# Kernel tuning notes

Measured on AMD Instinct MI355X. Metric: run time of the kernel, lower is better.

Reference implementation:

```python
import jax, jax.numpy as jnp
import numpy as np

# Module constants from init_kwargs
A, T, HID, H, EGO = 50, 50, 128, 32, 0
C = 4 * HID // H   # per-head out channels = 16
B = 32
NEG_SLOPE = 0.2    # PyG GATConv default negative_slope


def setup_inputs() -> dict:
    key = jax.random.key(0)
    k1, k2, k3, k4 = jax.random.split(key, 4)
    h = jax.random.normal(k1, (B, A, T, HID), dtype=jnp.float32)
    # GATConv params: lin.weight (H*C, HID), att_src/att_dst (H, C), bias (H*C,)
    W = jax.random.normal(k2, (H * C, HID), dtype=jnp.float32) * (1.0 / np.sqrt(HID))
    att_src = jax.random.normal(k3, (H, C), dtype=jnp.float32) * 0.1
    att_dst = jax.random.normal(k4, (H, C), dtype=jnp.float32) * 0.1
    bias = jnp.zeros((H * C,), dtype=jnp.float32)
    return {"h": h, "W": W, "att_src": att_src, "att_dst": att_dst, "bias": bias}


def reference(h, W, att_src, att_dst, bias):
    # h: (B, A, T, HID). Node id = t*A + a after permute, matching build_ego_star_edges.
    b = h.shape[0]
    x = jnp.transpose(h, (0, 2, 1, 3))                       # (B, T, A, HID)
    # Linear projection into heads: (B, T, A, H, C)
    xw = jnp.einsum('btad,hcd->btahc', x, W.reshape(H, C, HID))
    a_src = jnp.einsum('btahc,hc->btah', xw, att_src)        # per-node src logit
    a_dst = jnp.einsum('btahc,hc->btah', xw, att_dst)        # per-node dst logit

    # Star topology: every (t_src, a != EGO) node -> every (t_dst, EGO) node.
    ne = jnp.array([a for a in range(A) if a != EGO])        # (A-1,) non-ego agents
    S = T * (A - 1)                                          # neighbors per ego dst
    x_ne = xw[:, :, ne].reshape(b, S, H, C)                  # (B, S, H, C)
    a_src_ne = a_src[:, :, ne].reshape(b, S, H)              # (B, S, H)
    a_dst_ego = a_dst[:, :, EGO]                             # (B, T, H)

    # Per-edge attention logits, segment-softmax over the S neighbors of each dst.
    logits = jax.nn.leaky_relu(a_src_ne[:, None, :, :] + a_dst_ego[:, :, None, :],
                               negative_slope=NEG_SLOPE)     # (B, T, S, H)
    att = jax.nn.softmax(logits, axis=2)

    # Weighted aggregation: (B, T, H, C) -> flatten heads (concat=True)
    out_ego = jnp.einsum('btsh,bshc->bthc', att, x_ne).reshape(b, T, H * C)

    # Nodes with no incoming edges get zero aggregation; bias added to all.
    out = jnp.zeros((b, T, A, H * C), dtype=h.dtype).at[:, :, EGO].set(out_ego)
    out = out + bias
    return jnp.transpose(out, (0, 2, 1, 3))                  # (B, A, T, H*C)
```

## Files before the change

### kernel.cpp

```cpp
#include <hip/hip_runtime.h>
#include <math.h>

#define NA    50
#define NT    50
#define HIDK  128
#define NH    32
#define NC    16
#define NB    32
#define SAT   2500
#define NS    2450
#define NOUT  512

__global__ __launch_bounds__(256) void k0_pq(const float* __restrict__ W,
                                             const float* __restrict__ att_src,
                                             const float* __restrict__ att_dst,
                                             float* __restrict__ PQ) {
  int g = blockIdx.x * 256 + threadIdx.x;
  int j = g >> 7, k = g & 127;
  int hh = j & 31;
  const float* att = (j < 32) ? att_src : att_dst;
  float acc = 0.f;
  #pragma unroll
  for (int c = 0; c < 16; ++c)
    acc = fmaf(att[hh * 16 + c], W[(size_t)(hh * 16 + c) * 128 + k], acc);
  PQ[g] = acc;
}

__global__ __launch_bounds__(256) void k1_ud(
    const float* __restrict__ X,
    const float* __restrict__ PQ,
    float* __restrict__ u,
    float* __restrict__ dv)
{
  __shared__ float Ast[32][68];
  __shared__ float Bst[32][68];
  const int tid = threadIdx.x;
  const int m0 = blockIdx.x * 64;
  const int ty = tid >> 4, tx = tid & 15;
  float acc[4][4] = {};
  const int sr = tid >> 3, sc = tid & 7;

  for (int kc = 0; kc < 128; kc += 32) {
    #pragma unroll
    for (int L = 0; L < 2; ++L) {
      int row = sr + L * 32;
      float4 v = *(const float4*)&X[(size_t)(m0 + row) * 128 + kc + sc * 4];
      Ast[sc*4+0][row] = v.x; Ast[sc*4+1][row] = v.y;
      Ast[sc*4+2][row] = v.z; Ast[sc*4+3][row] = v.w;
      float4 w = *(const float4*)&PQ[(size_t)row * 128 + kc + sc * 4];
      Bst[sc*4+0][row] = w.x; Bst[sc*4+1][row] = w.y;
      Bst[sc*4+2][row] = w.z; Bst[sc*4+3][row] = w.w;
    }
    __syncthreads();
    #pragma unroll
    for (int k = 0; k < 32; ++k) {
      float4 a4 = *(const float4*)&Ast[k][ty * 4];
      float4 b4 = *(const float4*)&Bst[k][tx * 4];
      float a[4] = {a4.x, a4.y, a4.z, a4.w};
      float bb[4] = {b4.x, b4.y, b4.z, b4.w};
      #pragma unroll
      for (int i = 0; i < 4; ++i)
        #pragma unroll
        for (int j = 0; j < 4; ++j)
          acc[i][j] = fmaf(a[i], bb[j], acc[i][j]);
    }
    __syncthreads();
  }

  #pragma unroll
  for (int i = 0; i < 4; ++i) {
    int m = m0 + ty * 4 + i;
    int b = m / SAT, s = m - b * SAT;
    #pragma unroll
    for (int jj = 0; jj < 4; ++jj) {
      int col = tx * 4 + jj;
      if (col < 32)
        u[(size_t)(b * 32 + col) * SAT + s] = acc[i][jj];
      else if (s < NT)
        dv[(size_t)(b * 32 + col - 32) * NT + s] = acc[i][jj];
    }
  }
}

#define LOADG(B_, g_) do {                                                  \
    _Pragma("unroll")                                                       \
    for (int j = 0; j < 4; ++j) {                                           \
      int idx_ = base + 2 * ((g_) * 4 + j);                                 \
      e##B_[j] = sE[idx_]; s##B_[j] = sIdx[idx_];                           \
    }                                                                       \
    _Pragma("unroll")                                                       \
    for (int j = 0; j < 4; ++j)                                             \
      x##B_[j] = *(const float4*)(xb + (size_t)s##B_[j] * HIDK);            \
  } while (0)

#define COMPG(B_) do {                                                      \
    _Pragma("unroll")                                                       \
    for (int j = 0; j < 4; ++j) {                                           \
      float2 ee = e##B_[j]; float4 xx = x##B_[j];                           \
      a1[0]=fmaf(ee.x,xx.x,a1[0]); a1[1]=fmaf(ee.x,xx.y,a1[1]);             \
      a1[2]=fmaf(ee.x,xx.z,a1[2]); a1[3]=fmaf(ee.x,xx.w,a1[3]);             \
      a2[0]=fmaf(ee.y,xx.x,a2[0]); a2[1]=fmaf(ee.y,xx.y,a2[1]);             \
      a2[2]=fmaf(ee.y,xx.z,a2[2]); a2[3]=fmaf(ee.y,xx.w,a2[3]);             \
      z1 += ee.x; z2 += ee.y;                                               \
    }                                                                       \
  } while (0)

__global__ __launch_bounds__(512, 4) void k2_attn(
    const float* __restrict__ X,
    const float* __restrict__ u,
    const float* __restrict__ dv,
    const float* __restrict__ W,
    const float* __restrict__ bias,
    float* __restrict__ out)
{
  const int id = blockIdx.x;
  const int b  = (id & 7) + 8 * (id >> 8);
  const int h  = (id >> 3) & 31;
  const int tid = threadIdx.x;

  __shared__ float Bb[2][51][129];
  __shared__ float2 sE[NS];
  __shared__ unsigned short sIdx[NS];
  __shared__ float sTheta[50], sD[50], sF1[50], sF2[50];
  __shared__ int   sRank[50];
  __shared__ int   offs[52];
  __shared__ int   offCur[51];
  __shared__ int   segOrder[51];
  __shared__ int   segCtr;
  __shared__ float red[8];
  __shared__ float sMaxU;

  float* sU = &Bb[0][0][0];
  unsigned short* sBeta = (unsigned short*)&Bb[1][0][0];

  const size_t bh = (size_t)b * 32 + h;
  const float* uP = u + bh * SAT + NT;

  float mx = -1e30f;
  for (int i = tid; i < NS; i += 512) { float v = uP[i]; sU[i] = v; mx = fmaxf(mx, v); }
  if (tid < 50) sD[tid] = dv[bh * NT + tid];
  if (tid < 51) offCur[tid] = 0;
  #pragma unroll
  for (int o = 32; o; o >>= 1) mx = fmaxf(mx, __shfl_xor(mx, o));
  if ((tid & 63) == 0) red[tid >> 6] = mx;
  __syncthreads();
  if (tid == 0) {
    float m2 = red[0];
    #pragma unroll
    for (int k = 1; k < 8; ++k) m2 = fmaxf(m2, red[k]);
    sMaxU = m2;
  }
  __syncthreads();
  const float maxU = sMaxU;

  if (tid < 50) {
    float th = -sD[tid];
    int r = 0;
    for (int t2 = 0; t2 < 50; ++t2) {
      float th2 = -sD[t2];
      r += (th2 < th) || (th2 == th && t2 < tid);
    }
    sRank[tid] = r;
    sTheta[r] = th;
    float x = maxU + sD[tid];
    float L = (x >= 0.f) ? x : 0.2f * x;
    sF1[tid] = __expf(x - L);
    sF2[tid] = __expf(0.2f * x - L);
  }
  __syncthreads();

  for (int i = tid; i < NS; i += 512) {
    float uu = sU[i];
    int lo = 0, hi = 50;
    while (lo < hi) { int mid = (lo + hi) >> 1; if (sTheta[mid] <= uu) lo = mid + 1; else hi = mid; }
    sBeta[i] = (unsigned short)lo;
    atomicAdd(&offCur[lo], 1);
  }
  __syncthreads();

  if (tid < 64) {
    int c = (tid < 51) ? offCur[tid] : 0;
    int inc = c;
    #pragma unroll
    for (int o = 1; o < 64; o <<= 1) {
      int n = __shfl_up(inc, o);
      if (tid >= o) inc += n;
    }
    if (tid < 51) { int ex = inc - c; offs[tid] = ex; offCur[tid] = ex; }
    if (tid == 50) offs[51] = inc;
  }
  __syncthreads();

  if (tid < 51) {
    int sz = offs[tid + 1] - offs[tid];
    int r = 0;
    for (int t2 = 0; t2 < 51; ++t2) {
      int sz2 = offs[t2 + 1] - offs[t2];
      r += (sz2 > sz) || (sz2 == sz && t2 < tid);
    }
    segOrder[r] = tid;
  }
  if (tid == 511) segCtr = 0;
  for (int i = tid; i < NS; i += 512) {
    float uu = sU[i];
    int beta = sBeta[i];
    int pos = atomicAdd(&offCur[beta], 1);
    sE[pos] = make_float2(__expf(uu - maxU), __expf(0.2f * (uu - maxU)));
    sIdx[pos] = (unsigned short)(i + NT);
  }
  __syncthreads();

  {
    const int lane = tid & 63;
    const int slot = lane >> 5;
    const int cq   = lane & 31;
    const float* xb = X + (size_t)b * SAT * HIDK + cq * 4;

    for (;;) {
      int kidx = 0;
      if (lane == 0) kidx = atomicAdd(&segCtr, 1);
      kidx = __shfl(kidx, 0);
      if (kidx >= 51) break;
      const int seg = segOrder[kidx];

      const int i0 = offs[seg], i1 = offs[seg + 1];
      const int base = i0 + slot;
      int np = i1 - base;
      np = (np > 0) ? ((np + 1) >> 1) : 0;
      const int G = np >> 2;

      float a1[4] = {0.f, 0.f, 0.f, 0.f};
      float a2[4] = {0.f, 0.f, 0.f, 0.f};
      float z1 = 0.f, z2 = 0.f;

      float2 eA[4], eB[4]; int sA[4], sB[4]; float4 xA[4], xB[4];
      int g = 0;
      if (G) LOADG(A, 0);
      while (g + 2 <= G) {
        LOADG(B, g + 1);
        COMPG(A);
        if (g + 2 < G) LOADG(A, g + 2);
        COMPG(B);
        g += 2;
      }
      if (g < G) COMPG(A);
      for (int k = G * 4; k < np; ++k) {
        int idx = base + 2 * k;
        float2 ee = sE[idx];
        int ss = sIdx[idx];
        float4 xx = *(const float4*)(xb + (size_t)ss * HIDK);
        a1[0]=fmaf(ee.x,xx.x,a1[0]); a1[1]=fmaf(ee.x,xx.y,a1[1]);
        a1[2]=fmaf(ee.x,xx.z,a1[2]); a1[3]=fmaf(ee.x,xx.w,a1[3]);
        a2[0]=fmaf(ee.y,xx.x,a2[0]); a2[1]=fmaf(ee.y,xx.y,a2[1]);
        a2[2]=fmaf(ee.y,xx.z,a2[2]); a2[3]=fmaf(ee.y,xx.w,a2[3]);
        z1 += ee.x; z2 += ee.y;
      }

      #pragma unroll
      for (int j = 0; j < 4; ++j) {
        a1[j] += __shfl_xor(a1[j], 32);
        a2[j] += __shfl_xor(a2[j], 32);
      }
      z1 += __shfl_xor(z1, 32);
      z2 += __shfl_xor(z2, 32);
      if (slot == 0) {
        #pragma unroll
        for (int j = 0; j < 4; ++j) {
          Bb[0][seg][cq * 4 + j] = a1[j];
          Bb[1][seg][cq * 4 + j] = a2[j];
        }
        if (cq == 0) { Bb[0][seg][128] = z1; Bb[1][seg][128] = z2; }
      }
    }
  }
  __syncthreads();

  float* WshT = (float*)sE;
  const float* Wh = W + (size_t)h * 16 * 128;
  for (int v = tid; v < 2048; v += 512) {
    int k = v >> 4, cout = v & 15;
    WshT[k * 16 + cout] = Wh[(size_t)cout * 128 + k];
  }
  for (int task = tid; task < 258; task += 512) {
    int which = task >= 129;
    int c = task - which * 129;
    if (which == 0) {
      float run = 0.f;
      for (int k = 50; k >= 0; --k) { float tmp = Bb[0][k][c]; Bb[0][k][c] = run; run += tmp; }
    } else {
      float run = 0.f;
      for (int k = 0; k <= 50; ++k) { run += Bb[1][k][c]; Bb[1][k][c] = run; }
    }
  }
  __syncthreads();

  for (int task = tid; task < NT * NC; task += 512) {
    int t = task >> 4, cout = task & 15;
    int r = sRank[t];
    float F1 = sF1[t], F2 = sF2[t];
    float z = F1 * Bb[0][r][128] + F2 * Bb[1][r][128];
    const float* b1r = &Bb[0][r][0];
    const float* b2r = &Bb[1][r][0];
    float n1 = 0.f, n2 = 0.f;
    #pragma unroll 4
    for (int c = 0; c < 128; ++c) {
      float w = WshT[c * 16 + cout];
      n1 = fmaf(b1r[c], w, n1);
      n2 = fmaf(b2r[c], w, n2);
    }
    out[((size_t)b * SAT + t) * NOUT + h * 16 + cout] =
        (F1 * n1 + F2 * n2) / z + bias[h * 16 + cout];
  }

  {
    int g0 = id * 9800 + tid;
    const float4 b4 = ((const float4*)bias)[g0 & 127];
    float4* o4 = (float4*)out;
    int gEnd = (id + 1) * 9800;
    for (int g = g0; g < gEnd; g += 512) {
      int bb2 = g / 313600;
      int o = g - bb2 * 313600;
      o4[(size_t)bb2 * 320000 + 6400 + o] = b4;
    }
  }
}

extern "C" void kernel_launch(void* const* d_in, const int* in_sizes, int n_in,
                              void* d_out, int out_size, void* d_ws, size_t ws_size,
                              hipStream_t stream) {
  const float* X       = (const float*)d_in[0];
  const float* Wm      = (const float*)d_in[1];
  const float* att_src = (const float*)d_in[2];
  const float* att_dst = (const float*)d_in[3];
  const float* bias    = (const float*)d_in[4];
  float* out = (float*)d_out;

  float* PQ = (float*)d_ws;
  float* u  = PQ + 64 * 128;
  float* dv = u + (size_t)NB * NH * SAT;

  hipLaunchKernelGGL(k0_pq, dim3(32), dim3(256), 0, stream, Wm, att_src, att_dst, PQ);
  hipLaunchKernelGGL(k1_ud, dim3(1250), dim3(256), 0, stream, X, PQ, u, dv);
  hipLaunchKernelGGL(k2_attn, dim3(1024), dim3(512), 0, stream,
                     X, u, dv, Wm, bias, out);
}
```

Measured before the change: 289.6 us.

## Project segment partial sums through W before prefix scan

The per-segment 128-channel partial sums are now multiplied by the head's W slice first, giving 16 outputs plus the normalizer per segment. The suffix and prefix scans then run over 17 columns instead of 129, and the final per-t step becomes a cheap combine instead of a 128-long dot product per output. This relies on linearity of the scan and projection. The row stride is padded to 132 so rows can be read as float4, and W is read straight from global memory rather than first being transposed into shared memory.

```diff
diff --git a/kernel.cpp b/kernel.cpp
--- a/kernel.cpp
+++ b/kernel.cpp
@@ -82,6 +82,8 @@
   }
 }
 
+#define BBW 132
+
 #define LOADG(B_, g_) do {                                                  \
     _Pragma("unroll")                                                       \
     for (int j = 0; j < 4; ++j) {                                           \
@@ -104,6 +106,8 @@
       z1 += ee.x; z2 += ee.y;                                               \
     }                                                                       \
   } while (0)
+
+#define PP(s,k,c) Pa[(((s)*51+(k))*17)+(c)]
 
 __global__ __launch_bounds__(512, 4) void k2_attn(
     const float* __restrict__ X,
@@ -118,7 +122,7 @@
   const int h  = (id >> 3) & 31;
   const int tid = threadIdx.x;
 
-  __shared__ float Bb[2][51][129];
+  __shared__ float Bb[2][51][BBW];
   __shared__ float2 sE[NS];
   __shared__ unsigned short sIdx[NS];
   __shared__ float sTheta[50], sD[50], sF1[50], sF2[50];
@@ -132,6 +136,7 @@
 
   float* sU = &Bb[0][0][0];
   unsigned short* sBeta = (unsigned short*)&Bb[1][0][0];
+  float* Pa = (float*)sE;
 
   const size_t bh = (size_t)b * 32 + h;
   const float* uP = u + bh * SAT + NT;
@@ -275,21 +280,35 @@
   }
   __syncthreads();
 
-  float* WshT = (float*)sE;
-  const float* Wh = W + (size_t)h * 16 * 128;
-  for (int v = tid; v < 2048; v += 512) {
-    int k = v >> 4, cout = v & 15;
-    WshT[k * 16 + cout] = Wh[(size_t)cout * 128 + k];
-  }
-  for (int task = tid; task < 258; task += 512) {
-    int which = task >= 129;
-    int c = task - which * 129;
-    if (which == 0) {
+  for (int task = tid; task < 1734; task += 512) {
+    int s = task >= 867;
+    int rem = task - s * 867;
+    int k = rem / 17, cout = rem - k * 17;
+    if (cout == 16) {
+      PP(s, k, 16) = Bb[s][k][128];
+    } else {
+      const float4* br = (const float4*)&Bb[s][k][0];
+      const float4* wr = (const float4*)&W[(size_t)(h * 16 + cout) * 128];
+      float acc = 0.f;
+      #pragma unroll
+      for (int c4 = 0; c4 < 32; ++c4) {
+        float4 bv = br[c4], wv = wr[c4];
+        acc = fmaf(bv.x, wv.x, fmaf(bv.y, wv.y, fmaf(bv.z, wv.z, fmaf(bv.w, wv.w, acc))));
+      }
+      PP(s, k, cout) = acc;
+    }
+  }
+  __syncthreads();
+
+  if (tid < 34) {
+    int s = tid >= 17;
+    int cout = tid - s * 17;
+    if (s == 0) {
       float run = 0.f;
-      for (int k = 50; k >= 0; --k) { float tmp = Bb[0][k][c]; Bb[0][k][c] = run; run += tmp; }
+      for (int k = 50; k >= 0; --k) { float tmp = PP(0, k, cout); PP(0, k, cout) = run; run += tmp; }
     } else {
       float run = 0.f;
-      for (int k = 0; k <= 50; ++k) { run += Bb[1][k][c]; Bb[1][k][c] = run; }
+      for (int k = 0; k <= 50; ++k) { run += PP(1, k, cout); PP(1, k, cout) = run; }
     }
   }
   __syncthreads();
@@ -298,18 +317,9 @@
     int t = task >> 4, cout = task & 15;
     int r = sRank[t];
     float F1 = sF1[t], F2 = sF2[t];
-    float z = F1 * Bb[0][r][128] + F2 * Bb[1][r][128];
-    const float* b1r = &Bb[0][r][0];
-    const float* b2r = &Bb[1][r][0];
-    float n1 = 0.f, n2 = 0.f;
-    #pragma unroll 4
-    for (int c = 0; c < 128; ++c) {
-      float w = WshT[c * 16 + cout];
-      n1 = fmaf(b1r[c], w, n1);
-      n2 = fmaf(b2r[c], w, n2);
-    }
-    out[((size_t)b * SAT + t) * NOUT + h * 16 + cout] =
-        (F1 * n1 + F2 * n2) / z + bias[h * 16 + cout];
+    float z = F1 * PP(0, r, 16) + F2 * PP(1, r, 16);
+    float n = F1 * PP(0, r, cout) + F2 * PP(1, r, cout);
+    out[((size_t)b * SAT + t) * NOUT + h * 16 + cout] = n / z + bias[h * 16 + cout];
   }
 
   {
```

Measured after the change: 356.9 us. +23.2%, slower.

## Compute ego dst logits inside attention kernel, shrink projection GEMM to src only

Applied to the files above, without the earlier changes.

The projection GEMM previously produced 64 columns (32 src and 32 dst logits) for every node, even though dst logits are only needed for the 50 ego rows per batch. It now computes only the 32 src columns, using 128-row tiles that halve the grid. The attention kernel recomputes its 50 ego dst logits directly from X and the dst half of PQ with a small 8-lane dot product and shuffle reduction. This removes half the GEMM FLOPs and the dv buffer round-trip, in exchange for a little redundant work per (b,h) block.

```diff
diff --git a/kernel.cpp b/kernel.cpp
--- a/kernel.cpp
+++ b/kernel.cpp
@@ -26,30 +26,31 @@
   PQ[g] = acc;
 }
 
-__global__ __launch_bounds__(256) void k1_ud(
+__global__ __launch_bounds__(256) void k1_u(
     const float* __restrict__ X,
     const float* __restrict__ PQ,
-    float* __restrict__ u,
-    float* __restrict__ dv)
+    float* __restrict__ u)
 {
-  __shared__ float Ast[32][68];
-  __shared__ float Bst[32][68];
+  __shared__ float Ast[32][132];
+  __shared__ float Bst[32][36];
   const int tid = threadIdx.x;
-  const int m0 = blockIdx.x * 64;
-  const int ty = tid >> 4, tx = tid & 15;
+  const int m0 = blockIdx.x * 128;
+  const int ty = tid >> 3, tx = tid & 7;
   float acc[4][4] = {};
   const int sr = tid >> 3, sc = tid & 7;
 
   for (int kc = 0; kc < 128; kc += 32) {
     #pragma unroll
-    for (int L = 0; L < 2; ++L) {
+    for (int L = 0; L < 4; ++L) {
       int row = sr + L * 32;
       float4 v = *(const float4*)&X[(size_t)(m0 + row) * 128 + kc + sc * 4];
       Ast[sc*4+0][row] = v.x; Ast[sc*4+1][row] = v.y;
       Ast[sc*4+2][row] = v.z; Ast[sc*4+3][row] = v.w;
-      float4 w = *(const float4*)&PQ[(size_t)row * 128 + kc + sc * 4];
-      Bst[sc*4+0][row] = w.x; Bst[sc*4+1][row] = w.y;
-      Bst[sc*4+2][row] = w.z; Bst[sc*4+3][row] = w.w;
+    }
+    {
+      float4 w = *(const float4*)&PQ[(size_t)sr * 128 + kc + sc * 4];
+      Bst[sc*4+0][sr] = w.x; Bst[sc*4+1][sr] = w.y;
+      Bst[sc*4+2][sr] = w.z; Bst[sc*4+3][sr] = w.w;
     }
     __syncthreads();
     #pragma unroll
@@ -74,10 +75,7 @@
     #pragma unroll
     for (int jj = 0; jj < 4; ++jj) {
       int col = tx * 4 + jj;
-      if (col < 32)
-        u[(size_t)(b * 32 + col) * SAT + s] = acc[i][jj];
-      else if (s < NT)
-        dv[(size_t)(b * 32 + col - 32) * NT + s] = acc[i][jj];
+      u[(size_t)(b * 32 + col) * SAT + s] = acc[i][jj];
     }
   }
 }
@@ -108,7 +106,7 @@
 __global__ __launch_bounds__(512, 4) void k2_attn(
     const float* __restrict__ X,
     const float* __restrict__ u,
-    const float* __restrict__ dv,
+    const float* __restrict__ PQ,
     const float* __restrict__ W,
     const float* __restrict__ bias,
     float* __restrict__ out)
@@ -135,10 +133,25 @@
 
   const size_t bh = (size_t)b * 32 + h;
   const float* uP = u + bh * SAT + NT;
+  const float* Xb = X + (size_t)b * SAT * HIDK;
 
   float mx = -1e30f;
   for (int i = tid; i < NS; i += 512) { float v = uP[i]; sU[i] = v; mx = fmaxf(mx, v); }
-  if (tid < 50) sD[tid] = dv[bh * NT + tid];
+  if (tid < 400) {
+    int row = tid >> 3, l = tid & 7;
+    const float4* xr = (const float4*)(Xb + (size_t)row * HIDK + l * 16);
+    const float4* qr = (const float4*)(PQ + (size_t)(32 + h) * 128 + l * 16);
+    float acc = 0.f;
+    #pragma unroll
+    for (int c4 = 0; c4 < 4; ++c4) {
+      float4 x = xr[c4], q = qr[c4];
+      acc = fmaf(x.x, q.x, fmaf(x.y, q.y, fmaf(x.z, q.z, fmaf(x.w, q.w, acc))));
+    }
+    acc += __shfl_xor(acc, 1);
+    acc += __shfl_xor(acc, 2);
+    acc += __shfl_xor(acc, 4);
+    if (l == 0) sD[row] = acc;
+  }
   if (tid < 51) offCur[tid] = 0;
   #pragma unroll
   for (int o = 32; o; o >>= 1) mx = fmaxf(mx, __shfl_xor(mx, o));
@@ -214,7 +227,7 @@
     const int lane = tid & 63;
     const int slot = lane >> 5;
     const int cq   = lane & 31;
-    const float* xb = X + (size_t)b * SAT * HIDK + cq * 4;
+    const float* xb = Xb + cq * 4;
 
     for (;;) {
       int kidx = 0;
@@ -337,10 +350,9 @@
 
   float* PQ = (float*)d_ws;
   float* u  = PQ + 64 * 128;
-  float* dv = u + (size_t)NB * NH * SAT;
 
   hipLaunchKernelGGL(k0_pq, dim3(32), dim3(256), 0, stream, Wm, att_src, att_dst, PQ);
-  hipLaunchKernelGGL(k1_ud, dim3(1250), dim3(256), 0, stream, X, PQ, u, dv);
+  hipLaunchKernelGGL(k1_u, dim3(625), dim3(256), 0, stream, X, PQ, u);
   hipLaunchKernelGGL(k2_attn, dim3(1024), dim3(512), 0, stream,
-                     X, u, dv, Wm, bias, out);
+                     X, u, PQ, Wm, bias, out);
 }
```

After: 278.7 us. 1.04x faster.
